# Optimization experiments

Hardware: AMD Instinct MI355X
Metric: run time of the kernel (lower is better)

## Reference

```python
import jax, jax.numpy as jnp
import numpy as np


def conv_transpose_4s2p1(x, w, b):
    # torch ConvTranspose2d(k=4, s=2, p=1). w is torch layout [Cin, Cout, 4, 4].
    # Equivalent to a regular conv with lhs_dilation=2, per-side pad k-1-p=2,
    # spatially-flipped kernel and in/out channels swapped.
    wk = jnp.flip(w, (2, 3)).transpose(1, 0, 2, 3)  # [Cout, Cin, 4, 4]
    y = jax.lax.conv_general_dilated(
        x, wk, window_strides=(1, 1), padding=((2, 2), (2, 2)),
        lhs_dilation=(2, 2), dimension_numbers=('NCHW', 'OIHW', 'NCHW'))
    return y + b[None, :, None, None]


def pac_conv_transpose_3s1p1(y, guide, w, b):
    # PacConvTranspose2d(k=3, s=1, p=1): with stride 1 this equals pacconv2d on
    # input zero-padded by k-1-p = 1, with the weight in/out-permuted and flipped
    # (pacnet native impl). Adaptive kernel: K_kk = exp(-0.5*||g_nbr - g_center||^2)
    # computed on the (zero-padded) guide at output resolution.
    B, C, H, W = y.shape
    wk = jnp.flip(w, (2, 3)).transpose(1, 0, 2, 3)  # [Cout, Cin, 3, 3]
    Co = wk.shape[0]
    gp = jnp.pad(guide, ((0, 0), (0, 0), (1, 1), (1, 1)))
    yp = jnp.pad(y, ((0, 0), (0, 0), (1, 1), (1, 1)))
    out = jnp.zeros((B, Co, H, W), y.dtype)
    for i in range(3):  # fixed 3x3 taps, not a data-dim loop
        for j in range(3):
            gn = gp[:, :, i:i + H, j:j + W]                # [B,Cg,H,W] neighbor
            d = gn - guide
            k = jnp.exp(-0.5 * jnp.sum(d * d, axis=1))      # [B,H,W] gaussian kernel
            yn = yp[:, :, i:i + H, j:j + W]                # [B,C,H,W]
            out = out + jnp.einsum('oc,bchw->bohw', wk[:, :, i, j], yn * k[:, None])
    return out + b[None, :, None, None]


def setup_inputs() -> dict:
    key = jax.random.key(0)
    k1, k2, k3, k4, k5, k6 = jax.random.split(key, 6)
    B, Cin, Cout, H, W = 4, 256, 128, 64, 64
    x = jax.random.normal(k1, (B, Cin, H, W), jnp.float32)
    # guide scaled so ||diff||^2 over 128 channels stays O(1-10) and the
    # gaussian kernel is not numerically degenerate
    guide = 0.08 * jax.random.normal(k2, (B, Cout, 2 * H, 2 * W), jnp.float32)
    w1 = jax.random.normal(k3, (Cin, Cout, 4, 4), jnp.float32) / np.sqrt(Cin * 16)
    b1 = 0.01 * jax.random.normal(k4, (Cout,), jnp.float32)
    w2 = jax.random.normal(k5, (Cout, Cout, 3, 3), jnp.float32) / np.sqrt(Cout * 9)
    b2 = 0.01 * jax.random.normal(k6, (Cout,), jnp.float32)
    return {'x': x, 'guide': guide, 'w1': w1, 'b1': b1, 'w2': w2, 'b2': b2}


def reference(x, guide, w1, b1, w2, b2):
    y = conv_transpose_4s2p1(x, w1, b1)          # [B, Cout, 2H, 2W]
    out = pac_conv_transpose_3s1p1(y, guide, w2, b2)
    return out
```

## Files before the change

### kernel.cpp

```cpp
#include <hip/hip_runtime.h>

#define B_  4
#define C1  256
#define C2  128
#define HH  64
#define WW  64
#define H2  128
#define W2  128

using short8  = __attribute__((ext_vector_type(8))) short;
using floatx4 = __attribute__((ext_vector_type(4))) float;
typedef unsigned short ushort_t;

#define GLOBAL_AS __attribute__((address_space(1)))
#define LDS_AS    __attribute__((address_space(3)))

#define W1C_OFF 0u
#define W1C_ELEMS (4 * 4 * 128 * 256)
#define W2C_OFF (W1C_ELEMS * 2u)
#define W2C_ELEMS (9 * 128 * 128)
#define KG_OFF  (W2C_OFF + W2C_ELEMS * 2u)
#define KG_ELEMS (B_ * H2 * 9 * W2)
#define XT_OFF  (KG_OFF + KG_ELEMS * 4u)
#define XT_ELEMS (B_ * HH * WW * C1)
#define Y_OFF   (XT_OFF + XT_ELEMS * 2u)
#define Y_ELEMS (B_ * H2 * W2 * C2)

static __device__ __forceinline__ ushort_t f2bf(float f) {
    union { float f; unsigned u; } v; v.f = f;
    unsigned r = v.u + 0x7FFFu + ((v.u >> 16) & 1u);
    return (ushort_t)(r >> 16);
}

__global__ void w1c_kernel(const float* __restrict__ w1, ushort_t* __restrict__ w1c) {
    int i = blockIdx.x * 256 + threadIdx.x;
    const int ci  = i & 255;
    const int co  = (i >> 8) & 127;
    const int tap = (i >> 15) & 3;
    const int cls = i >> 17;
    const int kh  = (cls >> 1) + 2 * (tap >> 1);
    const int kw  = (cls & 1) + 2 * (tap & 1);
    w1c[i] = f2bf(w1[((ci * C2 + co) * 4 + kh) * 4 + kw]);
}

__global__ void w2c_kernel(const float* __restrict__ w2, ushort_t* __restrict__ w2c) {
    int i = blockIdx.x * 256 + threadIdx.x;
    const int ci  = i & 127;
    const int o   = (i >> 7) & 127;
    const int tap = i >> 14;
    const int fi  = 2 - tap / 3;
    const int fj  = 2 - tap % 3;
    const int gs  = ((((ci >> 3) ^ (o & 7)) << 3) | (ci & 7));
    w2c[tap * 16384 + o * 128 + gs] = f2bf(w2[((ci * C2 + o) * 3 + fi) * 3 + fj]);
}

__global__ __launch_bounds__(256) void xt_kernel(const float* __restrict__ x,
                                                 ushort_t* __restrict__ xT) {
    const int ih = blockIdx.x;
    const int b  = blockIdx.y;
    const int tid = threadIdx.x;
    __shared__ ushort_t tile[64 * 72];

    for (int chunk = 0; chunk < 4; ++chunk) {
        const int ci0 = chunk * 64;
        if (chunk) __syncthreads();
#pragma unroll
        for (int it = 0; it < 16; ++it) {
            const int cc = it * 4 + (tid >> 6);
            const int iw = tid & 63;
            const float v = x[(((size_t)b * C1 + ci0 + cc) * HH + ih) * WW + iw];
            tile[iw * 72 + cc] = f2bf(v);
        }
        __syncthreads();
#pragma unroll
        for (int it = 0; it < 2; ++it) {
            const int i  = it * 256 + tid;
            const int iw = i >> 3;
            const int t  = i & 7;
            const int4 v = *reinterpret_cast<const int4*>(&tile[iw * 72 + t * 8]);
            *reinterpret_cast<int4*>(&xT[(((size_t)(b * HH + ih) * WW) + iw) * C1 + ci0 + t * 8]) = v;
        }
    }
}

__global__ __launch_bounds__(512) void k_kernel(const float* __restrict__ guide,
                                                float* __restrict__ kg) {
    const int h = blockIdx.x;
    const int b = blockIdx.y;
    const int tid = threadIdx.x;
    const int cq  = tid >> 7;
    const int n   = tid & 127;

    float acc[9];
#pragma unroll
    for (int t = 0; t < 9; ++t) acc[t] = 0.f;

    const float* gb = guide + (size_t)b * C2 * H2 * W2;
    for (int c = cq * 32; c < cq * 32 + 32; ++c) {
        const float* grow = gb + (c * H2 + h) * W2;
        const float gc = grow[n];
#pragma unroll
        for (int di = 0; di < 3; ++di) {
            const int hh = h + di - 1;
            const bool rv = (hh >= 0) && (hh < H2);
            const float* gr = gb + (c * H2 + (rv ? hh : 0)) * W2;
#pragma unroll
            for (int dj = 0; dj < 3; ++dj) {
                const int col = n + dj - 1;
                const bool cv = rv && (col >= 0) && (col < W2);
                const float gn = cv ? gr[col] : 0.f;
                const float d = gn - gc;
                acc[di * 3 + dj] += d * d;
            }
        }
    }

    __shared__ float part[4][9][128];
#pragma unroll
    for (int t = 0; t < 9; ++t) part[cq][t][n] = acc[t];
    __syncthreads();

    for (int i = tid; i < 1152; i += 512) {
        const int t  = i >> 7;
        const int nn = i & 127;
        const float s = part[0][t][nn] + part[1][t][nn] + part[2][t][nn] + part[3][t][nn];
        kg[(size_t)(b * H2 + h) * 1152 + i] = __expf(-0.5f * s);
    }
}

__global__ __launch_bounds__(256, 2) void deconv_mfma(const ushort_t* __restrict__ xT,
                                                      const ushort_t* __restrict__ w1c,
                                                      const float* __restrict__ b1,
                                                      ushort_t* __restrict__ y) {
    const int pwc = blockIdx.x;
    const int pr  = blockIdx.y;
    const int b   = blockIdx.z;
    const int base_oh = (pr >> 1) * 4 + (pr & 1);
    const int p    = (base_oh + 1) & 1;
    const int ihA0 = (base_oh + 1 - p) >> 1;
    const int pwp  = 1 - pwc;
    const int cls  = p * 2 + pwp;

    const int tid  = threadIdx.x;
    const int lane = tid & 63;
    const int wave = tid >> 6;
    const int wm   = (wave & 1) * 64;
    const int wn   = (wave >> 1) * 64;
    const int quad = lane >> 4;
    const int l15  = lane & 15;

    __shared__ __align__(16) ushort_t lds[2 * 128 * 72];
    ushort_t* As = lds;
    ushort_t* Bs = lds + 128 * 72;

    floatx4 acc[4][4];
#pragma unroll
    for (int mi = 0; mi < 4; ++mi)
#pragma unroll
        for (int ni = 0; ni < 4; ++ni) acc[mi][ni] = (floatx4)0.f;

    for (int kc = 0; kc < 4; ++kc) {
        const int ci0 = kc * 64;
        for (int tap = 0; tap < 4; ++tap) {
            const int th = tap >> 1, tw = tap & 1;
            __syncthreads();
#pragma unroll
            for (int it = 0; it < 4; ++it) {
                const int i   = it * 256 + tid;
                const int row = i >> 3;
                const int t   = i & 7;
                const int4 v = *reinterpret_cast<const int4*>(
                    &w1c[((size_t)(cls * 4 + tap) * 128 + row) * 256 + ci0 + t * 8]);
                *reinterpret_cast<int4*>(&As[row * 72 + t * 8]) = v;
            }
#pragma unroll
            for (int it = 0; it < 4; ++it) {
                const int i   = it * 256 + tid;
                const int row = i >> 3;
                const int t   = i & 7;
                const int rh  = row >> 6;
                const int n64 = row & 63;
                const int ih  = ihA0 + rh - th;
                const int iw  = n64 + pwc - tw;
                int4 v = make_int4(0, 0, 0, 0);
                if (ih >= 0 && ih < HH && iw >= 0 && iw < WW)
                    v = *reinterpret_cast<const int4*>(
                        &xT[(((size_t)(b * HH + ih) * WW) + iw) * C1 + ci0 + t * 8]);
                *reinterpret_cast<int4*>(&Bs[row * 72 + t * 8]) = v;
            }
            __syncthreads();
#pragma unroll
            for (int k2 = 0; k2 < 2; ++k2) {
                short8 af[4], bfr[4];
#pragma unroll
                for (int mi = 0; mi < 4; ++mi)
                    af[mi] = *reinterpret_cast<const short8*>(
                        &As[(wm + mi * 16 + l15) * 72 + k2 * 32 + quad * 8]);
#pragma unroll
                for (int ni = 0; ni < 4; ++ni)
                    bfr[ni] = *reinterpret_cast<const short8*>(
                        &Bs[(wn + ni * 16 + l15) * 72 + k2 * 32 + quad * 8]);
#pragma unroll
                for (int mi = 0; mi < 4; ++mi)
#pragma unroll
                    for (int ni = 0; ni < 4; ++ni)
                        acc[mi][ni] = __builtin_amdgcn_mfma_f32_16x16x32_bf16(
                            af[mi], bfr[ni], acc[mi][ni], 0, 0, 0);
            }
        }
    }

    __syncthreads();
    ushort_t* Ot = lds;
#pragma unroll
    for (int mi = 0; mi < 4; ++mi)
#pragma unroll
        for (int ni = 0; ni < 4; ++ni) {
            const int n = wn + ni * 16 + l15;
#pragma unroll
            for (int r = 0; r < 4; ++r) {
                const int co = wm + mi * 16 + quad * 4 + r;
                Ot[n * 136 + co] = f2bf(acc[mi][ni][r] + b1[co]);
            }
        }
    __syncthreads();
#pragma unroll
    for (int it = 0; it < 8; ++it) {
        const int i   = it * 256 + tid;
        const int n   = i >> 4;
        const int t   = i & 15;
        const int rh  = n >> 6;
        const int n64 = n & 63;
        const int oh  = base_oh + 2 * rh;
        const int ow  = 2 * n64 + pwc;
        const int4 v = *reinterpret_cast<const int4*>(&Ot[n * 136 + t * 8]);
        *reinterpret_cast<int4*>(&y[(((size_t)(b * H2 + oh) * W2) + ow) * C2 + t * 8]) = v;
    }
}

__global__ __launch_bounds__(512, 2) void pac_mfma(const ushort_t* __restrict__ y,
                                                   const float* __restrict__ kg,
                                                   const ushort_t* __restrict__ w2c,
                                                   const float* __restrict__ b2,
                                                   float* __restrict__ out) {
    const int hblk = blockIdx.x;
    const int b    = blockIdx.y;
    const int h0   = hblk * 2;

    const int tid  = threadIdx.x;
    const int lane = tid & 63;
    const int wave = tid >> 6;
    const int rsub = wave >> 2;
    const int q    = wave & 3;
    const int wm   = (q & 1) * 64;
    const int wn   = (q >> 1) * 64;
    const int quad = lane >> 4;
    const int l15  = lane & 15;
    const int h    = h0 + rsub;

    __shared__ __align__(16) ushort_t SLAB[4][128 * 128];
    __shared__ __align__(16) ushort_t AS[128 * 128];

#pragma unroll 1
    for (int s = 0; s < 4; ++s) {
        const int hh = h0 - 1 + s;
        if (hh < 0 || hh >= H2) continue;
        const ushort_t* ysrc = y + (size_t)(b * H2 + hh) * W2 * C2;
#pragma unroll
        for (int it = 0; it < 4; ++it) {
            const int i = it * 512 + tid;
            const int w = i >> 4;
            const int c = i & 15;
            const int4 v = *reinterpret_cast<const int4*>(&ysrc[i * 8]);
            *reinterpret_cast<int4*>(&SLAB[s][w * 128 + ((c ^ (w & 7)) << 3)]) = v;
        }
    }
#pragma unroll
    for (int it = 0; it < 4; ++it) {
        const int i = it * 512 + tid;
        __builtin_amdgcn_global_load_lds((const GLOBAL_AS void*)(w2c + i * 8),
                                         (LDS_AS void*)(&AS[i * 8]), 16, 0, 0);
    }
    __syncthreads();

    float out_acc[4][4][4];
#pragma unroll
    for (int mi = 0; mi < 4; ++mi)
#pragma unroll
        for (int ni = 0; ni < 4; ++ni)
#pragma unroll
            for (int r = 0; r < 4; ++r) out_acc[mi][ni][r] = 0.f;

#pragma unroll 1
    for (int di = 0; di < 3; ++di) {
        const int hh  = h + di - 1;
        const bool hok = (hh >= 0) && (hh < H2);
        const ushort_t* SB = &SLAB[rsub + di][0];
#pragma unroll 1
        for (int dj = 0; dj < 3; ++dj) {
            const int tap = di * 3 + dj;

            float kv[4];
#pragma unroll
            for (int ni = 0; ni < 4; ++ni)
                kv[ni] = kg[(size_t)(b * H2 + h) * 1152 + tap * 128 + wn + ni * 16 + l15];

            floatx4 acc[4][4];
#pragma unroll
            for (int mi = 0; mi < 4; ++mi)
#pragma unroll
                for (int ni = 0; ni < 4; ++ni) acc[mi][ni] = (floatx4)0.f;

#pragma unroll
            for (int kc = 0; kc < 4; ++kc) {
                short8 af[4], bfr[4];
#pragma unroll
                for (int mi = 0; mi < 4; ++mi) {
                    const int row = wm + mi * 16 + l15;
                    af[mi] = *reinterpret_cast<const short8*>(
                        &AS[row * 128 + (((kc * 4 + quad) ^ (row & 7)) << 3)]);
                }
#pragma unroll
                for (int ni = 0; ni < 4; ++ni) {
                    const int col  = wn + ni * 16 + l15 + dj - 1;
                    const int colc = col & 127;
                    const short8 t = *reinterpret_cast<const short8*>(
                        &SB[colc * 128 + (((kc * 4 + quad) ^ (colc & 7)) << 3)]);
                    const bool ok = hok && (col >= 0) && (col < W2);
                    bfr[ni] = ok ? t : (short8)0;
                }
#pragma unroll
                for (int mi = 0; mi < 4; ++mi)
#pragma unroll
                    for (int ni = 0; ni < 4; ++ni)
                        acc[mi][ni] = __builtin_amdgcn_mfma_f32_16x16x32_bf16(
                            af[mi], bfr[ni], acc[mi][ni], 0, 0, 0);
            }
#pragma unroll
            for (int mi = 0; mi < 4; ++mi)
#pragma unroll
                for (int ni = 0; ni < 4; ++ni)
#pragma unroll
                    for (int r = 0; r < 4; ++r)
                        out_acc[mi][ni][r] += kv[ni] * acc[mi][ni][r];

            if (tap < 8) {
                __syncthreads();
                const ushort_t* wsrc = w2c + (size_t)(tap + 1) * 16384;
#pragma unroll
                for (int it = 0; it < 4; ++it) {
                    const int i = it * 512 + tid;
                    __builtin_amdgcn_global_load_lds((const GLOBAL_AS void*)(wsrc + i * 8),
                                                     (LDS_AS void*)(&AS[i * 8]), 16, 0, 0);
                }
                __syncthreads();
            }
        }
    }

#pragma unroll
    for (int mi = 0; mi < 4; ++mi)
#pragma unroll
        for (int ni = 0; ni < 4; ++ni) {
            const int w = wn + ni * 16 + l15;
#pragma unroll
            for (int r = 0; r < 4; ++r) {
                const int o = wm + mi * 16 + quad * 4 + r;
                out[(((size_t)b * C2 + o) * H2 + h) * W2 + w] = out_acc[mi][ni][r] + b2[o];
            }
        }
}

extern "C" void kernel_launch(void* const* d_in, const int* in_sizes, int n_in,
                              void* d_out, int out_size, void* d_ws, size_t ws_size,
                              hipStream_t stream) {
    const float* x     = (const float*)d_in[0];
    const float* guide = (const float*)d_in[1];
    const float* w1    = (const float*)d_in[2];
    const float* b1    = (const float*)d_in[3];
    const float* w2    = (const float*)d_in[4];
    const float* b2    = (const float*)d_in[5];
    float* out = (float*)d_out;

    ushort_t* w1c = (ushort_t*)((char*)d_ws + W1C_OFF);
    ushort_t* w2c = (ushort_t*)((char*)d_ws + W2C_OFF);
    float*    kg  = (float*)((char*)d_ws + KG_OFF);
    ushort_t* xT  = (ushort_t*)((char*)d_ws + XT_OFF);
    ushort_t* y   = (ushort_t*)((char*)d_ws + Y_OFF);

    w1c_kernel<<<W1C_ELEMS / 256, 256, 0, stream>>>(w1, w1c);
    w2c_kernel<<<W2C_ELEMS / 256, 256, 0, stream>>>(w2, w2c);
    xt_kernel<<<dim3(HH, B_), 256, 0, stream>>>(x, xT);
    k_kernel<<<dim3(H2, B_), 512, 0, stream>>>(guide, kg);
    deconv_mfma<<<dim3(2, 64, B_), 256, 0, stream>>>(xT, w1c, b1, y);
    pac_mfma<<<dim3(64, B_), 512, 0, stream>>>(y, kg, w2c, b2, out);
}
```

Baseline: 199.8 us.

## Restructure deconv kernel: stage input rows once in LDS and double-buffer weights

The transposed-conv MFMA kernel now runs 512 threads per block and covers both output column parities, so the two parity halves share one LDS copy of the three input rows they need (all 256 channels, XOR-swizzled). Weights are repacked into a swizzled per-phase layout and streamed into double-buffered LDS with direct global-to-LDS loads, overlapping the next weight tile's fetch with the current MFMAs. This removes the repeated per-tap global reloads of the activation tile and one barrier per phase. In exchange, LDS use per block rises substantially, which may limit how many blocks fit on a CU.

```diff
diff --git a/kernel.cpp b/kernel.cpp
--- a/kernel.cpp
+++ b/kernel.cpp
@@ -34,12 +34,16 @@
 
 __global__ void w1c_kernel(const float* __restrict__ w1, ushort_t* __restrict__ w1c) {
     int i = blockIdx.x * 256 + threadIdx.x;
-    const int ci  = i & 255;
-    const int co  = (i >> 8) & 127;
+    const int sub = i & 7;
+    const int gs  = (i >> 3) & 7;
+    const int co  = (i >> 6) & 127;
+    const int pwp = (i >> 13) & 1;
+    const int p   = (i >> 14) & 1;
     const int tap = (i >> 15) & 3;
-    const int cls = i >> 17;
-    const int kh  = (cls >> 1) + 2 * (tap >> 1);
-    const int kw  = (cls & 1) + 2 * (tap & 1);
+    const int kc  = (i >> 17) & 3;
+    const int ci  = kc * 64 + (((gs ^ (co & 7)) << 3) | sub);
+    const int kh  = p + 2 * (tap >> 1);
+    const int kw  = pwp + 2 * (tap & 1);
     w1c[i] = f2bf(w1[((ci * C2 + co) * 4 + kh) * 4 + kw]);
 }
 
@@ -128,30 +132,54 @@
     }
 }
 
-__global__ __launch_bounds__(256, 2) void deconv_mfma(const ushort_t* __restrict__ xT,
-                                                      const ushort_t* __restrict__ w1c,
+__global__ __launch_bounds__(512, 2) void deconv_mfma(const ushort_t* __restrict__ xT,
+                                                      const ushort_t* __restrict__ w1s,
                                                       const float* __restrict__ b1,
                                                       ushort_t* __restrict__ y) {
-    const int pwc = blockIdx.x;
-    const int pr  = blockIdx.y;
-    const int b   = blockIdx.z;
+    const int pr = blockIdx.x;
+    const int b  = blockIdx.y;
     const int base_oh = (pr >> 1) * 4 + (pr & 1);
     const int p    = (base_oh + 1) & 1;
     const int ihA0 = (base_oh + 1 - p) >> 1;
-    const int pwp  = 1 - pwc;
-    const int cls  = p * 2 + pwp;
 
     const int tid  = threadIdx.x;
     const int lane = tid & 63;
     const int wave = tid >> 6;
-    const int wm   = (wave & 1) * 64;
-    const int wn   = (wave >> 1) * 64;
+    const int pwc  = wave >> 2;
+    const int q    = wave & 3;
+    const int wm   = (q & 1) * 64;
+    const int wn   = (q >> 1) * 64;
     const int quad = lane >> 4;
     const int l15  = lane & 15;
-
-    __shared__ __align__(16) ushort_t lds[2 * 128 * 72];
-    ushort_t* As = lds;
-    ushort_t* Bs = lds + 128 * 72;
+    const int pwp  = 1 - pwc;
+
+    __shared__ __align__(16) ushort_t BS[3 * 64 * 256];
+    __shared__ __align__(16) ushort_t AS[2][2 * 128 * 64];
+
+    {
+        const ushort_t* src = w1s + (size_t)(0 * 2 + p) * 16384;
+#pragma unroll
+        for (int it = 0; it < 4; ++it) {
+            const int i = it * 512 + tid;
+            __builtin_amdgcn_global_load_lds((const GLOBAL_AS void*)(src + i * 8),
+                                             (LDS_AS void*)(&AS[0][i * 8]), 16, 0, 0);
+        }
+    }
+#pragma unroll
+    for (int it = 0; it < 12; ++it) {
+        const int i   = it * 512 + tid;
+        const int pix = i >> 5;
+        const int g   = i & 31;
+        const int sr  = pix >> 6;
+        const int iw  = pix & 63;
+        const int ih  = ihA0 - 1 + sr;
+        int4 v = make_int4(0, 0, 0, 0);
+        if (ih >= 0 && ih < HH)
+            v = *reinterpret_cast<const int4*>(
+                &xT[(((size_t)(b * HH + ih) * WW) + iw) * C1 + g * 8]);
+        *reinterpret_cast<int4*>(&BS[pix * 256 + ((g ^ (pix & 7)) << 3)]) = v;
+    }
+    __syncthreads();
 
     floatx4 acc[4][4];
 #pragma unroll
@@ -159,59 +187,53 @@
 #pragma unroll
         for (int ni = 0; ni < 4; ++ni) acc[mi][ni] = (floatx4)0.f;
 
-    for (int kc = 0; kc < 4; ++kc) {
-        const int ci0 = kc * 64;
-        for (int tap = 0; tap < 4; ++tap) {
-            const int th = tap >> 1, tw = tap & 1;
-            __syncthreads();
+#pragma unroll 1
+    for (int ph = 0; ph < 16; ++ph) {
+        const int kc  = ph >> 2;
+        const int tap = ph & 3;
+        const int cur = ph & 1;
+        if (ph < 15) {
+            const ushort_t* src = w1s + (size_t)((ph + 1) * 2 + p) * 16384;
 #pragma unroll
             for (int it = 0; it < 4; ++it) {
-                const int i   = it * 256 + tid;
-                const int row = i >> 3;
-                const int t   = i & 7;
-                const int4 v = *reinterpret_cast<const int4*>(
-                    &w1c[((size_t)(cls * 4 + tap) * 128 + row) * 256 + ci0 + t * 8]);
-                *reinterpret_cast<int4*>(&As[row * 72 + t * 8]) = v;
-            }
-#pragma unroll
-            for (int it = 0; it < 4; ++it) {
-                const int i   = it * 256 + tid;
-                const int row = i >> 3;
-                const int t   = i & 7;
-                const int rh  = row >> 6;
-                const int n64 = row & 63;
-                const int ih  = ihA0 + rh - th;
+                const int i = it * 512 + tid;
+                __builtin_amdgcn_global_load_lds((const GLOBAL_AS void*)(src + i * 8),
+                                                 (LDS_AS void*)(&AS[cur ^ 1][i * 8]), 16, 0, 0);
+            }
+        }
+        const int th = tap >> 1, tw = tap & 1;
+#pragma unroll
+        for (int k2 = 0; k2 < 2; ++k2) {
+            short8 af[4], bfr[4];
+#pragma unroll
+            for (int mi = 0; mi < 4; ++mi) {
+                const int row = wm + mi * 16 + l15;
+                af[mi] = *reinterpret_cast<const short8*>(
+                    &AS[cur][pwp * 8192 + row * 64 + (((k2 * 4 + quad) ^ (row & 7)) << 3)]);
+            }
+#pragma unroll
+            for (int ni = 0; ni < 4; ++ni) {
+                const int n   = wn + ni * 16 + l15;
+                const int rh  = n >> 6;
+                const int n64 = n & 63;
                 const int iw  = n64 + pwc - tw;
-                int4 v = make_int4(0, 0, 0, 0);
-                if (ih >= 0 && ih < HH && iw >= 0 && iw < WW)
-                    v = *reinterpret_cast<const int4*>(
-                        &xT[(((size_t)(b * HH + ih) * WW) + iw) * C1 + ci0 + t * 8]);
-                *reinterpret_cast<int4*>(&Bs[row * 72 + t * 8]) = v;
-            }
-            __syncthreads();
-#pragma unroll
-            for (int k2 = 0; k2 < 2; ++k2) {
-                short8 af[4], bfr[4];
-#pragma unroll
-                for (int mi = 0; mi < 4; ++mi)
-                    af[mi] = *reinterpret_cast<const short8*>(
-                        &As[(wm + mi * 16 + l15) * 72 + k2 * 32 + quad * 8]);
+                const int pix = (rh - th + 1) * 64 + (iw & 63);
+                const short8 t = *reinterpret_cast<const short8*>(
+                    &BS[pix * 256 + kc * 64 + (((k2 * 4 + quad) ^ (pix & 7)) << 3)]);
+                const bool ok = (iw >= 0) && (iw < WW);
+                bfr[ni] = ok ? t : (short8)0;
+            }
+#pragma unroll
+            for (int mi = 0; mi < 4; ++mi)
 #pragma unroll
                 for (int ni = 0; ni < 4; ++ni)
-                    bfr[ni] = *reinterpret_cast<const short8*>(
-                        &Bs[(wn + ni * 16 + l15) * 72 + k2 * 32 + quad * 8]);
-#pragma unroll
-                for (int mi = 0; mi < 4; ++mi)
-#pragma unroll
-                    for (int ni = 0; ni < 4; ++ni)
-                        acc[mi][ni] = __builtin_amdgcn_mfma_f32_16x16x32_bf16(
-                            af[mi], bfr[ni], acc[mi][ni], 0, 0, 0);
-            }
-        }
-    }
-
-    __syncthreads();
-    ushort_t* Ot = lds;
+                    acc[mi][ni] = __builtin_amdgcn_mfma_f32_16x16x32_bf16(
+                        af[mi], bfr[ni], acc[mi][ni], 0, 0, 0);
+        }
+        __syncthreads();
+    }
+
+    ushort_t* Ot = BS;
 #pragma unroll
     for (int mi = 0; mi < 4; ++mi)
 #pragma unroll
@@ -220,20 +242,22 @@
 #pragma unroll
             for (int r = 0; r < 4; ++r) {
                 const int co = wm + mi * 16 + quad * 4 + r;
-                Ot[n * 136 + co] = f2bf(acc[mi][ni][r] + b1[co]);
+                Ot[(pwc * 128 + n) * 136 + co] = f2bf(acc[mi][ni][r] + b1[co]);
             }
         }
     __syncthreads();
 #pragma unroll
     for (int it = 0; it < 8; ++it) {
-        const int i   = it * 256 + tid;
-        const int n   = i >> 4;
-        const int t   = i & 15;
-        const int rh  = n >> 6;
-        const int n64 = n & 63;
-        const int oh  = base_oh + 2 * rh;
-        const int ow  = 2 * n64 + pwc;
-        const int4 v = *reinterpret_cast<const int4*>(&Ot[n * 136 + t * 8]);
+        const int i    = it * 512 + tid;
+        const int n_   = i >> 4;
+        const int t    = i & 15;
+        const int half = n_ >> 7;
+        const int n    = n_ & 127;
+        const int rh   = n >> 6;
+        const int n64  = n & 63;
+        const int oh   = base_oh + 2 * rh;
+        const int ow   = 2 * n64 + half;
+        const int4 v = *reinterpret_cast<const int4*>(&Ot[n_ * 136 + t * 8]);
         *reinterpret_cast<int4*>(&y[(((size_t)(b * H2 + oh) * W2) + ow) * C2 + t * 8]) = v;
     }
 }
@@ -392,6 +416,6 @@
     w2c_kernel<<<W2C_ELEMS / 256, 256, 0, stream>>>(w2, w2c);
     xt_kernel<<<dim3(HH, B_), 256, 0, stream>>>(x, xT);
     k_kernel<<<dim3(H2, B_), 512, 0, stream>>>(guide, kg);
-    deconv_mfma<<<dim3(2, 64, B_), 256, 0, stream>>>(xT, w1c, b1, y);
+    deconv_mfma<<<dim3(64, B_), 512, 0, stream>>>(xT, w1c, b1, y);
     pac_mfma<<<dim3(64, B_), 512, 0, stream>>>(y, kg, w2c, b2, out);
 }
```

New measurement: 184.3 us. -7.8%, faster.
